# Performance work log

Hardware: AMD Instinct MI355X
Metric: run time of the kernel (lower is better)

Reference implementation:

```python
import jax, jax.numpy as jnp
import numpy as np

OBS_DIM = 64; ACT_DIM = 18; INTER = 64; COMMAND = 32
UNITS = ACT_DIM + COMMAND + INTER  # 114; neuron order: [motor, command, inter]
Q_HIDDEN = max(32, UNITS)
B, T = 2048, 64
ODE_UNFOLDS = 6
EPS = 1e-8


def _build_wiring(seed=0):
    """NCP sparse wiring: sensory->inter, inter->command, command recurrent, command->motor."""
    rng = np.random.default_rng(seed)
    adj = np.zeros((UNITS, UNITS), np.float32)   # [pre, post]
    sens = np.zeros((OBS_DIM, UNITS), np.float32)
    motor = np.arange(ACT_DIM)
    cmd = np.arange(ACT_DIM, ACT_DIM + COMMAND)
    inter = np.arange(ACT_DIM + COMMAND, UNITS)
    for s in range(OBS_DIM):
        for d in rng.choice(inter, size=8, replace=False):
            sens[s, d] = rng.choice([-1.0, 1.0])
    for i in inter:
        for d in rng.choice(cmd, size=8, replace=False):
            adj[i, d] = rng.choice([-1.0, 1.0])
    for _ in range(32):
        adj[rng.choice(cmd), rng.choice(cmd)] = rng.choice([-1.0, 1.0])
    for m in motor:
        for s in rng.choice(cmd, size=8, replace=False):
            adj[s, m] = rng.choice([-1.0, 1.0])
    return adj, sens


def setup_inputs() -> dict:
    key = jax.random.key(0)
    ks = jax.random.split(key, 16)
    adj, sens = _build_wiring()
    u = lambda k, shape, lo, hi: jax.random.uniform(k, shape, jnp.float32, lo, hi)
    return {
        "obs": jax.random.normal(ks[0], (B, T, OBS_DIM), jnp.float32),
        "hidden": jnp.zeros((B, UNITS), jnp.float32),
        "input_w": jnp.ones((OBS_DIM,), jnp.float32),
        "input_b": jnp.zeros((OBS_DIM,), jnp.float32),
        "sensory_w": u(ks[1], (OBS_DIM, UNITS), 0.001, 1.0),
        "sensory_mu": u(ks[2], (OBS_DIM, UNITS), 0.3, 0.8),
        "sensory_sigma": u(ks[3], (OBS_DIM, UNITS), 3.0, 8.0),
        "sensory_erev": jnp.asarray(sens),
        "sensory_mask": jnp.asarray(np.abs(sens)),
        "w": u(ks[4], (UNITS, UNITS), 0.001, 1.0),
        "mu": u(ks[5], (UNITS, UNITS), 0.3, 0.8),
        "sigma": u(ks[6], (UNITS, UNITS), 3.0, 8.0),
        "erev": jnp.asarray(adj),
        "mask": jnp.asarray(np.abs(adj)),
        "gleak": u(ks[7], (UNITS,), 0.001, 1.0),
        "vleak": u(ks[8], (UNITS,), -0.2, 0.2),
        "cm": u(ks[9], (UNITS,), 0.4, 0.6),
        "q_w1": jax.random.normal(ks[10], (UNITS, Q_HIDDEN), jnp.float32) / np.sqrt(UNITS).astype(np.float32),
        "q_b1": jnp.zeros((Q_HIDDEN,), jnp.float32),
        "q_w2": jax.random.normal(ks[11], (Q_HIDDEN, ACT_DIM), jnp.float32) / np.sqrt(Q_HIDDEN).astype(np.float32),
        "q_b2": jnp.zeros((ACT_DIM,), jnp.float32),
    }


def _ltc_forward(obs, hidden, input_w, input_b, sensory_w, sensory_mu, sensory_sigma,
                 sensory_erev, sensory_mask, w, mu, sigma, erev, mask, gleak, vleak, cm):
    sw = sensory_w * sensory_mask          # sparse sensory synapses (S, U)
    ww = w * mask                          # sparse recurrent synapses (U, U)
    cm_t = cm * ODE_UNFOLDS                # cm / (elapsed_time / ode_unfolds), elapsed_time = 1.0

    @jax.checkpoint
    def step(h, x):
        xi = x * input_w + input_b                                                    # (B, S) affine input map
        s_act = sw * jax.nn.sigmoid((xi[:, :, None] - sensory_mu) * sensory_sigma)    # (B, S, U)
        w_num_s = jnp.sum(s_act * sensory_erev, axis=1)                               # (B, U)
        w_den_s = jnp.sum(s_act, axis=1)                                              # (B, U)

        def unfold(v, _):
            act = ww * jax.nn.sigmoid((v[:, :, None] - mu) * sigma)                   # (B, U, U)
            num = cm_t * v + gleak * vleak + jnp.sum(act * erev, axis=1) + w_num_s
            den = cm_t + gleak + jnp.sum(act, axis=1) + w_den_s
            return num / (den + EPS), None

        v, _ = jax.lax.scan(unfold, h, None, length=ODE_UNFOLDS)
        return v, None

    h, _ = jax.lax.scan(step, hidden, jnp.swapaxes(obs, 0, 1))  # scan over time
    return h


def reference(obs, hidden, input_w, input_b, sensory_w, sensory_mu, sensory_sigma,
              sensory_erev, sensory_mask, w, mu, sigma, erev, mask, gleak, vleak, cm,
              q_w1, q_b1, q_w2, q_b2):
    h = _ltc_forward(obs, hidden, input_w, input_b, sensory_w, sensory_mu, sensory_sigma,
                     sensory_erev, sensory_mask, w, mu, sigma, erev, mask, gleak, vleak, cm)
    q = jax.nn.relu(h @ q_w1 + q_b1) @ q_w2 + q_b2  # Q-head over full hidden state
    return q, h
```

## Files before the change

### kernel.cpp

```cpp
#include <hip/hip_runtime.h>

#define UNITS   114
#define SDIM    64
#define ACT     18
#define TSTEPS  64

#define CR 13
#define CS 9
#define ER_CAP 704

#define LOG2E 1.4426950408889634f
#define EPS   1e-8f

typedef float v2f __attribute__((ext_vector_type(2)));
__device__ __forceinline__ v2f fma2(v2f a, v2f b, v2f c) {
  return __builtin_elementwise_fma(a, b, c);
}
__device__ __forceinline__ float bperm(int addr, float v) {
  return __int_as_float(__builtin_amdgcn_ds_bpermute(addr, __float_as_int(v)));
}
__device__ __forceinline__ float dperm(int addr, float v) {
  return __int_as_float(__builtin_amdgcn_ds_permute(addr, __float_as_int(v)));
}
__device__ __forceinline__ void wsync() {
  __builtin_amdgcn_fence(__ATOMIC_ACQ_REL, "wavefront");
  __builtin_amdgcn_wave_barrier();
}
__device__ __forceinline__ int canonLane(int u) { return (u >= 64) ? (u - 64) : u; }

__device__ __forceinline__ int kthSetBit(unsigned long long m, int k) {
  int pos = 0;
#pragma unroll
  for (int ww = 32; ww >= 1; ww >>= 1) {
    const unsigned long long lowMask = ((1ull << ww) - 1ull);
    const int c = __popcll(m & lowMask);
    if (k >= c) { k -= c; m >>= ww; pos += ww; }
  }
  return pos;
}

__global__ __launch_bounds__(64, 2) void ltc_fused(
    const float* __restrict__ obs,     const float* __restrict__ hidden,
    const float* __restrict__ input_w, const float* __restrict__ input_b,
    const float* __restrict__ sw, const float* __restrict__ smu,
    const float* __restrict__ ssg, const float* __restrict__ serev,
    const float* __restrict__ smask,
    const float* __restrict__ w, const float* __restrict__ mu,
    const float* __restrict__ sigma, const float* __restrict__ erev,
    const float* __restrict__ mask,
    const float* __restrict__ gleak, const float* __restrict__ vleak,
    const float* __restrict__ cm,
    const float* __restrict__ q_w1, const float* __restrict__ q_b1,
    const float* __restrict__ q_w2, const float* __restrict__ q_b2,
    float* __restrict__ out, int B)
{
  const int l = threadIdx.x, b = blockIdx.x;
  __shared__ float mirror[256];
  __shared__ short ePre[ER_CAP];
  __shared__ int offL[64], degL[64];
  __shared__ int pLane[64], pF0[64], pRole[64];
  __shared__ int contIdx[64], contOwn[64], splitRole[64], split2[64], ownP[128];
  __shared__ int rcv[64];
  char* mbase = (char*)mirror;

  mirror[l] = hidden[(size_t)b*UNITS + l];
  if (l < 50) mirror[64 + l] = hidden[(size_t)b*UNITS + 64 + l];
  const float iw = input_w[l], ibv = input_b[l];
  const float* ob = obs + (size_t)b*(TSTEPS*SDIM) + l;

  int d = 0;
  if (l < 50) {
    for (int base = 18; base < 114; base += 16) {
      float mv[16];
#pragma unroll
      for (int q = 0; q < 16; ++q) mv[q] = mask[(base + q)*UNITS + l];
#pragma unroll
      for (int q = 0; q < 16; ++q) d += (mv[q] != 0.f) ? 1 : 0;
    }
  }
  const int dregR = (l < 50) ? d : 0;
  degL[l] = dregR;
  int incl = dregR;
#pragma unroll
  for (int o = 1; o < 64; o <<= 1) { const int nn = __shfl_up(incl, o); if (l >= o) incl += nn; }
  offL[l] = incl - dregR;
  contIdx[l] = 0; contOwn[l] = 0; splitRole[l] = -1; split2[l] = 0;
  ownP[2*l] = -1; ownP[2*l+1] = -1;
  wsync();
  if (l < 50) {
    int o = incl - dregR;
    for (int base = 18; base < 114; base += 16) {
      float mv[16];
#pragma unroll
      for (int q = 0; q < 16; ++q) mv[q] = mask[(base + q)*UNITS + l];
#pragma unroll
      for (int q = 0; q < 16; ++q)
        if (mv[q] != 0.f) ePre[o++] = (short)(base + q);
    }
  }
  wsync();
  {
    int lam = 0, f = 0, pc = 0;
    for (int p = 0; p < 50; ++p) {
      const int dd = __shfl(dregR, p);
      if (pc == 2 || f == CR || dd > 3*CR - f) { ++lam; f = 0; pc = 0; }
      if (lam > 63) lam = 63;
      if (l == 0) { pLane[p] = lam; pF0[p] = f; pRole[p] = pc; ownP[2*lam + pc] = p; }
      const int owner = lam, role = pc; ++pc;
      const int take = dd < (CR - f) ? dd : (CR - f);
      f += take; int rem = dd - take;
      if (rem > 0) {
        if (l == 0) { splitRole[owner] = role; split2[owner] = (rem > CR) ? 1 : 0; }
        ++lam; if (lam > 63) lam = 63;
        if (l == 0) { contIdx[lam] = 1; contOwn[lam] = owner; }
        pc = 1;
        const int t2 = rem < CR ? rem : CR; f = t2; rem -= t2;
        if (rem > 0) {
          ++lam; if (lam > 63) lam = 63;
          if (l == 0) { contIdx[lam] = 2; contOwn[lam] = owner; }
          pc = 1; f = rem;
        }
      }
    }
  }
  wsync();
  int dAr = (contIdx[l] == 1) ? contOwn[l] : -1;
  int dBr = (contIdx[l] == 2) ? contOwn[l] : -1;
  rcv[l] = 0; wsync();
  if (dAr >= 0) rcv[dAr] = 1;
  wsync();
  { const unsigned long long rM = __ballot(rcv[l] != 0), dM = __ballot(dAr < 0);
    if (dAr < 0) dAr = kthSetBit(~rM, __popcll(dM & ((1ull << l) - 1ull))); }
  wsync();
  rcv[l] = 0; wsync();
  if (dBr >= 0) rcv[dBr] = 1;
  wsync();
  { const unsigned long long rM = __ballot(rcv[l] != 0), dM = __ballot(dBr < 0);
    if (dBr < 0) dBr = kthSetBit(~rM, __popcll(dM & ((1ull << l) - 1ull))); }
  const int rPush1 = dAr * 4, rPush2 = dBr * 4;
  const float s1Ar = (splitRole[l] == 0) ? 1.f : 0.f, s1Br = (splitRole[l] == 1) ? 1.f : 0.f;
  const float s2r  = split2[l] ? 1.f : 0.f;
  const v2f gR1A = {s1Ar, s1Ar}, gR1B = {s1Br, s1Br};
  const v2f gR2A = {s1Ar*s2r, s1Ar*s2r}, gR2B = {s1Br*s2r, s1Br*s2r};
  const int uA = ownP[2*l], uB = ownP[2*l+1];
  const int rWrA = ((uA >= 0) ? uA : 128 + l) * 4;
  const int rWrB = ((uB >= 0) ? uB : 192 + l) * 4;
  const int rUA = (uA >= 0) ? uA : 0, rUB = (uB >= 0) ? uB : 0;
  float rNS[CR], rMS[CR]; v2f rWA[CR], rWB[CR]; int rad[CR];
  {
    const int ci = contIdx[l];
    int p1 = -1, base1 = 0, cnt1 = 0;
    if (ci) {
      const int o = contOwn[l];
      p1 = ownP[2*o + splitRole[o]];
      const int br = (CR - pF0[p1]) + ((ci == 2) ? CR : 0);
      base1 = offL[p1] + br;
      cnt1 = degL[p1] - br; if (cnt1 > CR) cnt1 = CR;
    }
    int fA = 0, tA = -1, oAo = 0;
    if (uA >= 0) { fA = pF0[uA]; const int rm = CR - fA; const int dd = degL[uA];
                   tA = dd < rm ? dd : rm; oAo = offL[uA]; }
    int fB = 0, tB = -1, oBo = 0;
    if (uB >= 0) { fB = pF0[uB]; const int rm = CR - fB; const int dd = degL[uB];
                   tB = dd < rm ? dd : rm; oBo = offL[uB]; }
#pragma unroll
    for (int s = 0; s < CR; ++s) {
      int e = -1, post = 0, isB = 0;
      if (ci && s < cnt1)                          { e = base1 + s;      post = p1; }
      else if (uA >= 0 && s >= fA && s < fA + tA)  { e = oAo + (s - fA); post = uA; }
      else if (uB >= 0 && s >= fB && s < fB + tB)  { e = oBo + (s - fB); post = uB; isB = 1; }
      if (e >= 0) {
        const int pre = (int)ePre[e];
        const int idx = pre * UNITS + post;
        const float sg_ = sigma[idx];
        rNS[s] = -sg_ * LOG2E; rMS[s] = mu[idx] * sg_ * LOG2E;
        const float wd = w[idx], wn = wd * erev[idx];
        rWA[s] = isB ? (v2f){0.f, 0.f} : (v2f){wn, wd};
        rWB[s] = isB ? (v2f){wn, wd} : (v2f){0.f, 0.f};
        rad[s] = pre * 4;
      } else {
        rNS[s] = 0.f; rMS[s] = 0.f;
        rWA[s] = (v2f){0.f, 0.f}; rWB[s] = (v2f){0.f, 0.f};
        rad[s] = 0;
      }
    }
  }
  wsync();

  int ds_ = 0;
  {
    const int col = 50 + l;
    for (int base = 0; base < 64; base += 16) {
      float mv[16];
#pragma unroll
      for (int q = 0; q < 16; ++q) mv[q] = smask[(base + q)*UNITS + col];
#pragma unroll
      for (int q = 0; q < 16; ++q) ds_ += (mv[q] != 0.f) ? 1 : 0;
    }
  }
  const int dregS = ds_;
  degL[l] = dregS;
  int inclS = dregS;
#pragma unroll
  for (int o = 1; o < 64; o <<= 1) { const int nn = __shfl_up(inclS, o); if (l >= o) inclS += nn; }
  offL[l] = inclS - dregS;
  contIdx[l] = 0; contOwn[l] = 0; splitRole[l] = -1; split2[l] = 0;
  ownP[2*l] = -1; ownP[2*l+1] = -1;
  wsync();
  {
    int o = inclS - dregS; const int col = 50 + l;
    for (int base = 0; base < 64; base += 16) {
      float mv[16];
#pragma unroll
      for (int q = 0; q < 16; ++q) mv[q] = smask[(base + q)*UNITS + col];
#pragma unroll
      for (int q = 0; q < 16; ++q)
        if (mv[q] != 0.f) ePre[o++] = (short)(base + q);
    }
  }
  wsync();
  {
    int lam = 0, f = 0, pc = 0;
    for (int p = 0; p < 64; ++p) {
      const int dd = __shfl(dregS, p);
      if (pc == 2 || f == CS || dd > 3*CS - f) { ++lam; f = 0; pc = 0; }
      if (lam > 63) lam = 63;
      if (l == 0) { pLane[p] = lam; pF0[p] = f; pRole[p] = pc; ownP[2*lam + pc] = p; }
      const int owner = lam, role = pc; ++pc;
      const int take = dd < (CS - f) ? dd : (CS - f);
      f += take; int rem = dd - take;
      if (rem > 0) {
        if (l == 0) { splitRole[owner] = role; split2[owner] = (rem > CS) ? 1 : 0; }
        ++lam; if (lam > 63) lam = 63;
        if (l == 0) { contIdx[lam] = 1; contOwn[lam] = owner; }
        pc = 1;
        const int t2 = rem < CS ? rem : CS; f = t2; rem -= t2;
        if (rem > 0) {
          ++lam; if (lam > 63) lam = 63;
          if (l == 0) { contIdx[lam] = 2; contOwn[lam] = owner; }
          pc = 1; f = rem;
        }
      }
    }
  }
  wsync();
  int dAs = (contIdx[l] == 1) ? contOwn[l] : -1;
  int dBs = (contIdx[l] == 2) ? contOwn[l] : -1;
  rcv[l] = 0; wsync();
  if (dAs >= 0) rcv[dAs] = 1;
  wsync();
  { const unsigned long long rM = __ballot(rcv[l] != 0), dM = __ballot(dAs < 0);
    if (dAs < 0) dAs = kthSetBit(~rM, __popcll(dM & ((1ull << l) - 1ull))); }
  wsync();
  rcv[l] = 0; wsync();
  if (dBs >= 0) rcv[dBs] = 1;
  wsync();
  { const unsigned long long rM = __ballot(rcv[l] != 0), dM = __ballot(dBs < 0);
    if (dBs < 0) dBs = kthSetBit(~rM, __popcll(dM & ((1ull << l) - 1ull))); }
  wsync();
  int rAs = (ownP[2*l]   >= 0) ? canonLane(50 + ownP[2*l])   : -1;
  int rBs = (ownP[2*l+1] >= 0) ? canonLane(50 + ownP[2*l+1]) : -1;
  rcv[l] = 0; wsync();
  if (rAs >= 0) rcv[rAs] = 1;
  wsync();
  const int isRcvA = rcv[l];
  { const unsigned long long rM = __ballot(isRcvA != 0), dM = __ballot(rAs < 0);
    if (rAs < 0) rAs = kthSetBit(~rM, __popcll(dM & ((1ull << l) - 1ull))); }
  wsync();
  rcv[l] = 0; wsync();
  if (rBs >= 0) rcv[rBs] = 1;
  wsync();
  { const unsigned long long rM = __ballot(rcv[l] != 0), dM = __ballot(rBs < 0);
    if (rBs < 0) rBs = kthSetBit(~rM, __popcll(dM & ((1ull << l) - 1ull))); }
  const int sPush1 = dAs * 4, sPush2 = dBs * 4;
  const float s1As = (splitRole[l] == 0) ? 1.f : 0.f, s1Bs = (splitRole[l] == 1) ? 1.f : 0.f;
  const float s2s  = split2[l] ? 1.f : 0.f;
  const v2f gS1A = {s1As, s1As}, gS1B = {s1Bs, s1Bs};
  const v2f gS2A = {s1As*s2s, s1As*s2s}, gS2B = {s1Bs*s2s, s1Bs*s2s};
  const int sRtA = rAs * 4, sRtB = rBs * 4;
  const float sRndA = isRcvA ? 1.f : 0.f, sRndB = isRcvA ? 0.f : 1.f;
  const int pAs = ownP[2*l], pBs = ownP[2*l+1];
  const int sUA = (pAs >= 0) ? 50 + pAs : 0;
  const int sUB = (pBs >= 0) ? 50 + pBs : 0;
  float sNS[CS], sMS[CS]; v2f sWA[CS], sWB[CS]; int sad[CS];
  {
    const int ci = contIdx[l];
    int p1 = -1, base1 = 0, cnt1 = 0;
    if (ci) {
      const int o = contOwn[l];
      p1 = ownP[2*o + splitRole[o]];
      const int br = (CS - pF0[p1]) + ((ci == 2) ? CS : 0);
      base1 = offL[p1] + br;
      cnt1 = degL[p1] - br; if (cnt1 > CS) cnt1 = CS;
    }
    int fA = 0, tA = -1, oAo = 0;
    if (pAs >= 0) { fA = pF0[pAs]; const int rm = CS - fA; const int dd = degL[pAs];
                    tA = dd < rm ? dd : rm; oAo = offL[pAs]; }
    int fB = 0, tB = -1, oBo = 0;
    if (pBs >= 0) { fB = pF0[pBs]; const int rm = CS - fB; const int dd = degL[pBs];
                    tB = dd < rm ? dd : rm; oBo = offL[pBs]; }
#pragma unroll
    for (int s = 0; s < CS; ++s) {
      int e = -1, post = 0, isB = 0;
      if (ci && s < cnt1)                           { e = base1 + s;      post = p1;  }
      else if (pAs >= 0 && s >= fA && s < fA + tA)  { e = oAo + (s - fA); post = pAs; }
      else if (pBs >= 0 && s >= fB && s < fB + tB)  { e = oBo + (s - fB); post = pBs; isB = 1; }
      if (e >= 0) {
        const int pre = (int)ePre[e];
        const int idx = pre * UNITS + 50 + post;
        const float sg_ = ssg[idx];
        sNS[s] = -sg_ * LOG2E; sMS[s] = smu[idx] * sg_ * LOG2E;
        const float wd = sw[idx], wn = wd * serev[idx];
        sWA[s] = isB ? (v2f){0.f, 0.f} : (v2f){wn, wd};
        sWB[s] = isB ? (v2f){wn, wd} : (v2f){0.f, 0.f};
        sad[s] = pre * 4;
      } else {
        sNS[s] = 0.f; sMS[s] = 0.f;
        sWA[s] = (v2f){0.f, 0.f}; sWB[s] = (v2f){0.f, 0.f};
        sad[s] = 0;
      }
    }
  }

  const float cmA  = cm[rUA]*6.f, glvA  = gleak[rUA]*vleak[rUA], cgA  = cm[rUA]*6.f + gleak[rUA] + EPS;
  const float cmB  = cm[rUB]*6.f, glvB  = gleak[rUB]*vleak[rUB], cgB  = cm[rUB]*6.f + gleak[rUB] + EPS;
  const float cmSA = cm[sUA]*6.f, glvSA = gleak[sUA]*vleak[sUA], cgSA = cm[sUA]*6.f + gleak[sUA] + EPS;
  const float cmSB = cm[sUB]*6.f, glvSB = gleak[sUB]*vleak[sUB], cgSB = cm[sUB]*6.f + gleak[sUB] + EPS;

  const bool ownA  = (rWrA < 512), ownB  = (rWrB < 512);
  const bool ownSA = (sUA != 0),   ownSB = (sUB != 0);
  const v2f initRA = ownA  ? (v2f){glvA,  cgA}  : (v2f){0.f, EPS};
  const v2f initRB = ownB  ? (v2f){glvB,  cgB}  : (v2f){0.f, EPS};
  const v2f initSA = ownSA ? (v2f){glvSA, cgSA} : (v2f){0.f, EPS};
  const v2f initSB = ownSB ? (v2f){glvSB, cgSB} : (v2f){0.f, EPS};

  const int  iUnit = (l < 50) ? 64 + l : l;
  const int  iWr   = iUnit * 4;
  float vIn = hidden[(size_t)b*UNITS + iUnit];
  float vPA = hidden[(size_t)b*UNITS + rUA];
  float vPB = hidden[(size_t)b*UNITS + rUB];

  float aI, bI;
  {
    const float xi = fmaf(ob[0], iw, ibv);
    float uu[CS];
#pragma unroll
    for (int s = 0; s < CS; ++s) {
      float z = fmaf(bperm(sad[s], xi), sNS[s], sMS[s]);
      z = fminf(z, 30.f);
      uu[s] = 1.f + __builtin_amdgcn_exp2f(z);
    }
    float sg[CS];
#pragma unroll
    for (int q = 0; q < 4; ++q) {
      const float p = uu[2*q] * uu[2*q+1];
      const float r = __builtin_amdgcn_rcpf(p);
      sg[2*q]   = uu[2*q+1] * r;
      sg[2*q+1] = uu[2*q]   * r;
    }
    sg[8] = __builtin_amdgcn_rcpf(uu[8]);
    v2f cA = {0.f,0.f}, cB = {0.f,0.f};
#pragma unroll
    for (int s = 0; s < CS; ++s) {
      const v2f s2 = {sg[s], sg[s]};
      cA = fma2(sWA[s], s2, cA);
      cB = fma2(sWB[s], s2, cB);
    }
    const v2f m1 = {dperm(sPush1, cA.x), dperm(sPush1, cA.y)};
    const v2f m2 = {dperm(sPush2, cA.x), dperm(sPush2, cA.y)};
    v2f tA = fma2(gS1A, m1, cA); tA = fma2(gS2A, m2, tA);
    v2f tB = fma2(gS1B, m1, cB); tB = fma2(gS2B, m2, tB);
    const float rdA = __builtin_amdgcn_rcpf(cgSA + tA.y);
    const float aA = cmSA * rdA, bA = (glvSA + tA.x) * rdA;
    const float rdB = __builtin_amdgcn_rcpf(cgSB + tB.y);
    const float aB = cmSB * rdB, bB = (glvSB + tB.x) * rdB;
    const float ra1 = dperm(sRtA, aA), rb1 = dperm(sRtA, bA);
    const float ra2 = dperm(sRtB, aB), rb2 = dperm(sRtB, bB);
    aI = sRndA*ra1 + sRndB*ra2;
    bI = sRndA*rb1 + sRndB*rb2;
  }

  float xiN = fmaf(ob[SDIM], iw, ibv);
  float xrC = ob[2*SDIM];
  float su[CS];
  v2f acA = initSA, acB = initSB;
  v2f tSA = {0.f,0.f}, tSB = {0.f,0.f};
  float aIn = 0.f, bIn = 0.f;

  auto unfold = [&](auto chunk) {
    wsync();
    float uu[CR];
#pragma unroll
    for (int s = 0; s < CR; ++s) {
      const float pv = *(const float*)(mbase + rad[s]);
      const float z = fmaf(pv, rNS[s], rMS[s]);
      uu[s] = 1.f + __builtin_amdgcn_exp2f(z);
    }
    chunk();
    float sg[CR];
#pragma unroll
    for (int q = 0; q < 5; ++q) {
      const float p = uu[2*q] * uu[2*q+1];
      const float r = __builtin_amdgcn_rcpf(p);
      sg[2*q]   = uu[2*q+1] * r;
      sg[2*q+1] = uu[2*q]   * r;
    }
    {
      const float p01 = uu[10]*uu[11];
      const float r = __builtin_amdgcn_rcpf(p01*uu[12]);
      const float t12 = uu[12]*r;
      sg[10] = uu[11]*t12; sg[11] = uu[10]*t12; sg[12] = p01*r;
    }
    v2f a0 = initRA, a1 = {0.f,0.f}, b0 = initRB, b1 = {0.f,0.f};
#pragma unroll
    for (int s = 0; s < CR; ++s) {
      const v2f s2 = {sg[s], sg[s]};
      if (s & 1) { a1 = fma2(rWA[s], s2, a1); b1 = fma2(rWB[s], s2, b1); }
      else       { a0 = fma2(rWA[s], s2, a0); b0 = fma2(rWB[s], s2, b0); }
    }
    v2f aA = a0 + a1, aB = b0 + b1;
    const v2f m1 = {dperm(rPush1, aA.x), dperm(rPush1, aA.y)};
    const v2f m2 = {dperm(rPush2, aA.x), dperm(rPush2, aA.y)};
    v2f tA = fma2(gR1A, m1, aA); tA = fma2(gR2A, m2, tA);
    v2f tB = fma2(gR1B, m1, aB); tB = fma2(gR2B, m2, tB);
    const float dAq = tA.y, dBq = tB.y;
    const float rr = __builtin_amdgcn_rcpf(dAq * dBq);
    vPA = fmaf(cmA, vPA, tA.x) * (dBq * rr);
    vPB = fmaf(cmB, vPB, tB.x) * (dAq * rr);
    vIn = fmaf(aI, vIn, bI);
    wsync();
    *(float*)(mbase + rWrA) = vPA;
    *(float*)(mbase + rWrB) = vPB;
    *(float*)(mbase + iWr)  = vIn;
  };

  auto sExp = [&](int s) {
    float z = fmaf(bperm(sad[s], xiN), sNS[s], sMS[s]);
    z = fminf(z, 30.f);
    su[s] = 1.f + __builtin_amdgcn_exp2f(z);
  };
  auto sPair = [&](int s0) {
    const float p = su[s0] * su[s0+1];
    const float r = __builtin_amdgcn_rcpf(p);
    const float g0 = su[s0+1] * r, g1 = su[s0] * r;
    acA = fma2(sWA[s0],   (v2f){g0,g0}, acA);
    acA = fma2(sWA[s0+1], (v2f){g1,g1}, acA);
    acB = fma2(sWB[s0],   (v2f){g0,g0}, acB);
    acB = fma2(sWB[s0+1], (v2f){g1,g1}, acB);
  };

#pragma unroll 1
  for (int t = 0; t < TSTEPS; ++t) {
    unfold([&]{ sExp(0); sExp(1); });
    unfold([&]{ sExp(2); sExp(3); sPair(0); });
    unfold([&]{ sExp(4); sExp(5); sPair(2); });
    unfold([&]{ sExp(6); sExp(7); sExp(8); sPair(4); });
    unfold([&]{
      const float p67 = su[6] * su[7];
      const float r = __builtin_amdgcn_rcpf(p67 * su[8]);
      const float t67 = su[8] * r;
      const float g6 = su[7]*t67, g7 = su[6]*t67, g8 = p67*r;
      acA = fma2(sWA[6], (v2f){g6,g6}, acA); acB = fma2(sWB[6], (v2f){g6,g6}, acB);
      acA = fma2(sWA[7], (v2f){g7,g7}, acA); acB = fma2(sWB[7], (v2f){g7,g7}, acB);
      acA = fma2(sWA[8], (v2f){g8,g8}, acA); acB = fma2(sWB[8], (v2f){g8,g8}, acB);
      const v2f m1 = {dperm(sPush1, acA.x), dperm(sPush1, acA.y)};
      const v2f m2 = {dperm(sPush2, acA.x), dperm(sPush2, acA.y)};
      tSA = fma2(gS1A, m1, acA); tSA = fma2(gS2A, m2, tSA);
      tSB = fma2(gS1B, m1, acB); tSB = fma2(gS2B, m2, tSB);
    });
    unfold([&]{
      const float dA_ = tSA.y, dB_ = tSB.y;
      const float rr = __builtin_amdgcn_rcpf(dA_ * dB_);
      const float rdA = dB_ * rr, rdB = dA_ * rr;
      const float aA = cmSA * rdA, bA = tSA.x * rdA;
      const float aB = cmSB * rdB, bB = tSB.x * rdB;
      const float ra1 = dperm(sRtA, aA), rb1 = dperm(sRtA, bA);
      const float ra2 = dperm(sRtB, aB), rb2 = dperm(sRtB, bB);
      aIn = sRndA*ra1 + sRndB*ra2;
      bIn = sRndA*rb1 + sRndB*rb2;
    });
    aI = aIn; bI = bIn;
    xiN = fmaf(xrC, iw, ibv);
    const int tn = (t + 3 < TSTEPS) ? (t + 3) : (TSTEPS - 1);
    xrC = ob[tn * SDIM];
    acA = initSA; acB = initSB;
  }
  wsync();

  float* __restrict__ outH = out + (size_t)B * ACT;
  outH[(size_t)b*UNITS + l] = mirror[l];
  if (l < 50) outH[(size_t)b*UNITS + 64 + l] = mirror[64 + l];

  const int j2 = (l < 50) ? 64 + l : l;
  float h1 = q_b1[l], h2 = q_b1[j2];
  for (int i = 0; i < UNITS; ++i) {
    const float hv = mirror[i];
    h1 = fmaf(hv, q_w1[i*UNITS + l],  h1);
    h2 = fmaf(hv, q_w1[i*UNITS + j2], h2);
  }
  h1 = fmaxf(h1, 0.f); h2 = fmaxf(h2, 0.f);
  wsync();
  mirror[l] = h1;
  if (l < 50) mirror[64 + l] = h2;
  wsync();
  if (l < ACT) {
    float q = q_b2[l];
    for (int i = 0; i < UNITS; ++i) q = fmaf(mirror[i], q_w2[i*ACT + l], q);
    out[(size_t)b*ACT + l] = q;
  }
}

extern "C" void kernel_launch(void* const* d_in, const int* in_sizes, int n_in,
                              void* d_out, int out_size, void* d_ws, size_t ws_size,
                              hipStream_t stream)
{
  const float* obs           = (const float*)d_in[0];
  const float* hidden        = (const float*)d_in[1];
  const float* input_w       = (const float*)d_in[2];
  const float* input_b       = (const float*)d_in[3];
  const float* sensory_w     = (const float*)d_in[4];
  const float* sensory_mu    = (const float*)d_in[5];
  const float* sensory_sigma = (const float*)d_in[6];
  const float* sensory_erev  = (const float*)d_in[7];
  const float* sensory_mask  = (const float*)d_in[8];
  const float* w             = (const float*)d_in[9];
  const float* mu            = (const float*)d_in[10];
  const float* sigma         = (const float*)d_in[11];
  const float* erev          = (const float*)d_in[12];
  const float* mask          = (const float*)d_in[13];
  const float* gleak         = (const float*)d_in[14];
  const float* vleak         = (const float*)d_in[15];
  const float* cm            = (const float*)d_in[16];
  const float* q_w1          = (const float*)d_in[17];
  const float* q_b1          = (const float*)d_in[18];
  const float* q_w2          = (const float*)d_in[19];
  const float* q_b2          = (const float*)d_in[20];

  const int B = in_sizes[0] / (TSTEPS * SDIM);
  ltc_fused<<<B, 64, 0, stream>>>(
      obs, hidden, input_w, input_b,
      sensory_w, sensory_mu, sensory_sigma, sensory_erev, sensory_mask,
      w, mu, sigma, erev, mask,
      gleak, vleak, cm,
      q_w1, q_b1, q_w2, q_b2,
      (float*)d_out, B);
}
```

Measured before the change: 388.4 us.

## Hoist sparse wiring table construction into a separate prep kernel

The per-block setup that scans the masks, partitions edges across lanes and gathers per-edge parameters moves into a small 8-block prep kernel that writes packed per-lane tables and metadata to workspace. The main kernel now only loads these precomputed tables instead of every one of the 2048 blocks redoing the mask scans, prefix sums and assignment loops. The cost is an extra kernel launch and a global-memory dependency between the two kernels. Edge lists are now rebuilt from bitmasks with kthSetBit rather than stored in a shared-memory list.

```diff
diff --git a/kernel.cpp b/kernel.cpp
--- a/kernel.cpp
+++ b/kernel.cpp
@@ -7,7 +7,7 @@
 
 #define CR 13
 #define CS 9
-#define ER_CAP 704
+#define MSTRIDE 24
 
 #define LOG2E 1.4426950408889634f
 #define EPS   1e-8f
@@ -38,289 +38,306 @@
   }
   return pos;
 }
-
-__global__ __launch_bounds__(64, 2) void ltc_fused(
-    const float* __restrict__ obs,     const float* __restrict__ hidden,
-    const float* __restrict__ input_w, const float* __restrict__ input_b,
+__device__ __forceinline__ unsigned long long shfl_u64(unsigned long long v, int src) {
+  const int lo = __shfl((int)(unsigned)(v & 0xffffffffull), src);
+  const int hi = __shfl((int)(unsigned)(v >> 32), src);
+  return ((unsigned long long)(unsigned)hi << 32) | (unsigned)lo;
+}
+
+__global__ __launch_bounds__(64) void build_all(
+    const float* __restrict__ w,  const float* __restrict__ mu,
+    const float* __restrict__ sigma, const float* __restrict__ erev,
+    const float* __restrict__ mask,
     const float* __restrict__ sw, const float* __restrict__ smu,
     const float* __restrict__ ssg, const float* __restrict__ serev,
     const float* __restrict__ smask,
-    const float* __restrict__ w, const float* __restrict__ mu,
-    const float* __restrict__ sigma, const float* __restrict__ erev,
-    const float* __restrict__ mask,
-    const float* __restrict__ gleak, const float* __restrict__ vleak,
+    float4* __restrict__ recP4, float2* __restrict__ recP2, int* __restrict__ recAd,
+    float4* __restrict__ senP4, float2* __restrict__ senP2, int* __restrict__ senAd,
+    int* __restrict__ meta)
+{
+  const int l = threadIdx.x;
+  const int bid = blockIdx.x;
+  __shared__ int degL[64], pF0L[64];
+  __shared__ int contIdx[64], contOwn[64], splitRole[64], split2[64], ownP[128];
+  __shared__ int rcv[64];
+
+  contIdx[l] = 0; contOwn[l] = 0; splitRole[l] = -1; split2[l] = 0;
+  ownP[2*l] = -1; ownP[2*l+1] = -1;
+
+  if (bid < 4) {
+    unsigned long long cLo = 0ull, cHi = 0ull;
+    if (l < 50) {
+      for (int base = 0; base < 64; base += 16) {
+        float mv[16];
+#pragma unroll
+        for (int q = 0; q < 16; ++q) mv[q] = mask[(18 + base + q)*UNITS + l];
+#pragma unroll
+        for (int q = 0; q < 16; ++q) if (mv[q] != 0.f) cLo |= (1ull << (base + q));
+      }
+      for (int base = 0; base < 32; base += 16) {
+        float mv[16];
+#pragma unroll
+        for (int q = 0; q < 16; ++q) mv[q] = mask[(82 + base + q)*UNITS + l];
+#pragma unroll
+        for (int q = 0; q < 16; ++q) if (mv[q] != 0.f) cHi |= (1ull << (base + q));
+      }
+    }
+    const int dreg = __popcll(cLo) + __popcll(cHi);
+    degL[l] = dreg;
+    wsync();
+    {
+      int lam = 0, f = 0, pc = 0;
+      for (int p = 0; p < 50; ++p) {
+        const int dd = __shfl(dreg, p);
+        if (pc == 2 || f == CR || dd > 3*CR - f) { ++lam; f = 0; pc = 0; }
+        if (lam > 63) lam = 63;
+        if (l == 0) { pF0L[p] = f; ownP[2*lam + pc] = p; }
+        const int owner = lam, role = pc; ++pc;
+        const int take = dd < (CR - f) ? dd : (CR - f);
+        f += take; int rem = dd - take;
+        if (rem > 0) {
+          if (l == 0) { splitRole[owner] = role; split2[owner] = (rem > CR) ? 1 : 0; }
+          ++lam; if (lam > 63) lam = 63;
+          if (l == 0) { contIdx[lam] = 1; contOwn[lam] = owner; }
+          pc = 1;
+          const int t2 = rem < CR ? rem : CR; f = t2; rem -= t2;
+          if (rem > 0) {
+            ++lam; if (lam > 63) lam = 63;
+            if (l == 0) { contIdx[lam] = 2; contOwn[lam] = owner; }
+            pc = 1; f = rem;
+          }
+        }
+      }
+    }
+    wsync();
+    int dAr = (contIdx[l] == 1) ? contOwn[l] : -1;
+    int dBr = (contIdx[l] == 2) ? contOwn[l] : -1;
+    rcv[l] = 0; wsync();
+    if (dAr >= 0) rcv[dAr] = 1;
+    wsync();
+    { const unsigned long long rM = __ballot(rcv[l] != 0), dM = __ballot(dAr < 0);
+      if (dAr < 0) dAr = kthSetBit(~rM, __popcll(dM & ((1ull << l) - 1ull))); }
+    wsync();
+    rcv[l] = 0; wsync();
+    if (dBr >= 0) rcv[dBr] = 1;
+    wsync();
+    { const unsigned long long rM = __ballot(rcv[l] != 0), dM = __ballot(dBr < 0);
+      if (dBr < 0) dBr = kthSetBit(~rM, __popcll(dM & ((1ull << l) - 1ull))); }
+    const int uA = ownP[2*l], uB = ownP[2*l+1];
+    if (bid == 0) {
+      int* M = meta + l * MSTRIDE;
+      M[0] = dAr * 4; M[1] = dBr * 4;
+      const float s1A = (splitRole[l] == 0) ? 1.f : 0.f, s1B = (splitRole[l] == 1) ? 1.f : 0.f;
+      M[2] = __float_as_int(s1A); M[3] = __float_as_int(s1B);
+      const float s2 = split2[l] ? 1.f : 0.f;
+      M[4] = __float_as_int(s1A * s2); M[5] = __float_as_int(s1B * s2);
+      M[6] = ((uA >= 0) ? uA : 128 + l) * 4;
+      M[7] = ((uB >= 0) ? uB : 192 + l) * 4;
+      M[8] = (uA >= 0) ? uA : 0;
+      M[9] = (uB >= 0) ? uB : 0;
+    }
+    const int ci = contIdx[l];
+    int p1 = -1, br = 0, cnt1 = 0;
+    if (ci) {
+      const int o = contOwn[l];
+      p1 = ownP[2*o + splitRole[o]];
+      br = (CR - pF0L[p1]) + ((ci == 2) ? CR : 0);
+      cnt1 = degL[p1] - br; if (cnt1 > CR) cnt1 = CR;
+    }
+    int fA = 0, tA = -1;
+    if (uA >= 0) { fA = pF0L[uA]; const int rm = CR - fA; const int dd = degL[uA]; tA = dd < rm ? dd : rm; }
+    int fB = 0, tB = -1;
+    if (uB >= 0) { fB = pF0L[uB]; const int rm = CR - fB; const int dd = degL[uB]; tB = dd < rm ? dd : rm; }
+    for (int s = bid; s < CR; s += 4) {
+      int post = -1, rank = 0, isB = 0;
+      if (ci && s < cnt1)                          { post = p1; rank = br + s; }
+      else if (uA >= 0 && s >= fA && s < fA + tA)  { post = uA; rank = s - fA; }
+      else if (uB >= 0 && s >= fB && s < fB + tB)  { post = uB; rank = s - fB; isB = 1; }
+      const int postc = (post >= 0) ? post : 0;
+      const unsigned long long plo = shfl_u64(cLo, postc);
+      const unsigned long long phi = shfl_u64(cHi, postc);
+      float4 p4 = make_float4(0.f, 0.f, 0.f, 0.f);
+      float2 p2 = make_float2(0.f, 0.f);
+      int ad = 0;
+      if (post >= 0) {
+        const int c = __popcll(plo);
+        const int pre = (rank < c) ? (18 + kthSetBit(plo, rank)) : (82 + kthSetBit(phi, rank - c));
+        const int idx = pre * UNITS + post;
+        const float sg_ = sigma[idx];
+        const float nsgl = -sg_ * LOG2E, msl = mu[idx] * sg_ * LOG2E;
+        const float wd = w[idx], wn = wd * erev[idx];
+        p4 = make_float4(nsgl, msl, isB ? 0.f : wn, isB ? 0.f : wd);
+        p2 = isB ? make_float2(wn, wd) : make_float2(0.f, 0.f);
+        ad = pre * 4;
+      }
+      recP4[s*64 + l] = p4; recP2[s*64 + l] = p2; recAd[s*64 + l] = ad;
+    }
+  } else {
+    unsigned long long cS = 0ull;
+    {
+      const int col = 50 + l;
+      for (int base = 0; base < 64; base += 16) {
+        float mv[16];
+#pragma unroll
+        for (int q = 0; q < 16; ++q) mv[q] = smask[(base + q)*UNITS + col];
+#pragma unroll
+        for (int q = 0; q < 16; ++q) if (mv[q] != 0.f) cS |= (1ull << (base + q));
+      }
+    }
+    const int dreg = __popcll(cS);
+    degL[l] = dreg;
+    wsync();
+    {
+      int lam = 0, f = 0, pc = 0;
+      for (int p = 0; p < 64; ++p) {
+        const int dd = __shfl(dreg, p);
+        if (pc == 2 || f == CS || dd > 3*CS - f) { ++lam; f = 0; pc = 0; }
+        if (lam > 63) lam = 63;
+        if (l == 0) { pF0L[p] = f; ownP[2*lam + pc] = p; }
+        const int owner = lam, role = pc; ++pc;
+        const int take = dd < (CS - f) ? dd : (CS - f);
+        f += take; int rem = dd - take;
+        if (rem > 0) {
+          if (l == 0) { splitRole[owner] = role; split2[owner] = (rem > CS) ? 1 : 0; }
+          ++lam; if (lam > 63) lam = 63;
+          if (l == 0) { contIdx[lam] = 1; contOwn[lam] = owner; }
+          pc = 1;
+          const int t2 = rem < CS ? rem : CS; f = t2; rem -= t2;
+          if (rem > 0) {
+            ++lam; if (lam > 63) lam = 63;
+            if (l == 0) { contIdx[lam] = 2; contOwn[lam] = owner; }
+            pc = 1; f = rem;
+          }
+        }
+      }
+    }
+    wsync();
+    int dAs = (contIdx[l] == 1) ? contOwn[l] : -1;
+    int dBs = (contIdx[l] == 2) ? contOwn[l] : -1;
+    rcv[l] = 0; wsync();
+    if (dAs >= 0) rcv[dAs] = 1;
+    wsync();
+    { const unsigned long long rM = __ballot(rcv[l] != 0), dM = __ballot(dAs < 0);
+      if (dAs < 0) dAs = kthSetBit(~rM, __popcll(dM & ((1ull << l) - 1ull))); }
+    wsync();
+    rcv[l] = 0; wsync();
+    if (dBs >= 0) rcv[dBs] = 1;
+    wsync();
+    { const unsigned long long rM = __ballot(rcv[l] != 0), dM = __ballot(dBs < 0);
+      if (dBs < 0) dBs = kthSetBit(~rM, __popcll(dM & ((1ull << l) - 1ull))); }
+    wsync();
+    int rAs = (ownP[2*l]   >= 0) ? canonLane(50 + ownP[2*l])   : -1;
+    int rBs = (ownP[2*l+1] >= 0) ? canonLane(50 + ownP[2*l+1]) : -1;
+    rcv[l] = 0; wsync();
+    if (rAs >= 0) rcv[rAs] = 1;
+    wsync();
+    const int isRcvA = rcv[l];
+    { const unsigned long long rM = __ballot(isRcvA != 0), dM = __ballot(rAs < 0);
+      if (rAs < 0) rAs = kthSetBit(~rM, __popcll(dM & ((1ull << l) - 1ull))); }
+    wsync();
+    rcv[l] = 0; wsync();
+    if (rBs >= 0) rcv[rBs] = 1;
+    wsync();
+    { const unsigned long long rM = __ballot(rcv[l] != 0), dM = __ballot(rBs < 0);
+      if (rBs < 0) rBs = kthSetBit(~rM, __popcll(dM & ((1ull << l) - 1ull))); }
+    const int pAs = ownP[2*l], pBs = ownP[2*l+1];
+    if (bid == 4) {
+      int* M = meta + l * MSTRIDE;
+      M[10] = dAs * 4; M[11] = dBs * 4;
+      const float s1A = (splitRole[l] == 0) ? 1.f : 0.f, s1B = (splitRole[l] == 1) ? 1.f : 0.f;
+      M[12] = __float_as_int(s1A); M[13] = __float_as_int(s1B);
+      const float s2 = split2[l] ? 1.f : 0.f;
+      M[14] = __float_as_int(s1A * s2); M[15] = __float_as_int(s1B * s2);
+      M[16] = rAs * 4; M[17] = rBs * 4;
+      M[18] = __float_as_int(isRcvA ? 1.f : 0.f);
+      M[19] = __float_as_int(isRcvA ? 0.f : 1.f);
+      M[20] = (pAs >= 0) ? 50 + pAs : 0;
+      M[21] = (pBs >= 0) ? 50 + pBs : 0;
+    }
+    const int ci = contIdx[l];
+    int p1 = -1, br = 0, cnt1 = 0;
+    if (ci) {
+      const int o = contOwn[l];
+      p1 = ownP[2*o + splitRole[o]];
+      br = (CS - pF0L[p1]) + ((ci == 2) ? CS : 0);
+      cnt1 = degL[p1] - br; if (cnt1 > CS) cnt1 = CS;
+    }
+    int fA = 0, tA = -1;
+    if (pAs >= 0) { fA = pF0L[pAs]; const int rm = CS - fA; const int dd = degL[pAs]; tA = dd < rm ? dd : rm; }
+    int fB = 0, tB = -1;
+    if (pBs >= 0) { fB = pF0L[pBs]; const int rm = CS - fB; const int dd = degL[pBs]; tB = dd < rm ? dd : rm; }
+    for (int s = bid - 4; s < CS; s += 4) {
+      int post = -1, rank = 0, isB = 0;
+      if (ci && s < cnt1)                            { post = p1;  rank = br + s; }
+      else if (pAs >= 0 && s >= fA && s < fA + tA)   { post = pAs; rank = s - fA; }
+      else if (pBs >= 0 && s >= fB && s < fB + tB)   { post = pBs; rank = s - fB; isB = 1; }
+      const int postc = (post >= 0) ? post : 0;
+      const unsigned long long pm = shfl_u64(cS, postc);
+      float4 p4 = make_float4(0.f, 0.f, 0.f, 0.f);
+      float2 p2 = make_float2(0.f, 0.f);
+      int ad = 0;
+      if (post >= 0) {
+        const int pre = kthSetBit(pm, rank);
+        const int idx = pre * UNITS + 50 + post;
+        const float sg_ = ssg[idx];
+        const float nsgl = -sg_ * LOG2E, msl = smu[idx] * sg_ * LOG2E;
+        const float wd = sw[idx], wn = wd * serev[idx];
+        p4 = make_float4(nsgl, msl, isB ? 0.f : wn, isB ? 0.f : wd);
+        p2 = isB ? make_float2(wn, wd) : make_float2(0.f, 0.f);
+        ad = pre * 4;
+      }
+      senP4[s*64 + l] = p4; senP2[s*64 + l] = p2; senAd[s*64 + l] = ad;
+    }
+  }
+}
+
+__global__ __launch_bounds__(64, 2) void ltc_run(
+    const float* __restrict__ obs,     const float* __restrict__ hidden,
+    const float* __restrict__ input_w, const float* __restrict__ input_b,
+    const float* __restrict__ gleak,   const float* __restrict__ vleak,
     const float* __restrict__ cm,
     const float* __restrict__ q_w1, const float* __restrict__ q_b1,
     const float* __restrict__ q_w2, const float* __restrict__ q_b2,
-    float* __restrict__ out, int B)
+    const float4* __restrict__ recP4, const float2* __restrict__ recP2,
+    const int* __restrict__ recAd,
+    const float4* __restrict__ senP4, const float2* __restrict__ senP2,
+    const int* __restrict__ senAd,
+    const int* __restrict__ meta, float* __restrict__ out, int B)
 {
   const int l = threadIdx.x, b = blockIdx.x;
   __shared__ float mirror[256];
-  __shared__ short ePre[ER_CAP];
-  __shared__ int offL[64], degL[64];
-  __shared__ int pLane[64], pF0[64], pRole[64];
-  __shared__ int contIdx[64], contOwn[64], splitRole[64], split2[64], ownP[128];
-  __shared__ int rcv[64];
   char* mbase = (char*)mirror;
 
-  mirror[l] = hidden[(size_t)b*UNITS + l];
-  if (l < 50) mirror[64 + l] = hidden[(size_t)b*UNITS + 64 + l];
-  const float iw = input_w[l], ibv = input_b[l];
-  const float* ob = obs + (size_t)b*(TSTEPS*SDIM) + l;
-
-  int d = 0;
-  if (l < 50) {
-    for (int base = 18; base < 114; base += 16) {
-      float mv[16];
-#pragma unroll
-      for (int q = 0; q < 16; ++q) mv[q] = mask[(base + q)*UNITS + l];
-#pragma unroll
-      for (int q = 0; q < 16; ++q) d += (mv[q] != 0.f) ? 1 : 0;
-    }
-  }
-  const int dregR = (l < 50) ? d : 0;
-  degL[l] = dregR;
-  int incl = dregR;
-#pragma unroll
-  for (int o = 1; o < 64; o <<= 1) { const int nn = __shfl_up(incl, o); if (l >= o) incl += nn; }
-  offL[l] = incl - dregR;
-  contIdx[l] = 0; contOwn[l] = 0; splitRole[l] = -1; split2[l] = 0;
-  ownP[2*l] = -1; ownP[2*l+1] = -1;
-  wsync();
-  if (l < 50) {
-    int o = incl - dregR;
-    for (int base = 18; base < 114; base += 16) {
-      float mv[16];
-#pragma unroll
-      for (int q = 0; q < 16; ++q) mv[q] = mask[(base + q)*UNITS + l];
-#pragma unroll
-      for (int q = 0; q < 16; ++q)
-        if (mv[q] != 0.f) ePre[o++] = (short)(base + q);
-    }
-  }
-  wsync();
-  {
-    int lam = 0, f = 0, pc = 0;
-    for (int p = 0; p < 50; ++p) {
-      const int dd = __shfl(dregR, p);
-      if (pc == 2 || f == CR || dd > 3*CR - f) { ++lam; f = 0; pc = 0; }
-      if (lam > 63) lam = 63;
-      if (l == 0) { pLane[p] = lam; pF0[p] = f; pRole[p] = pc; ownP[2*lam + pc] = p; }
-      const int owner = lam, role = pc; ++pc;
-      const int take = dd < (CR - f) ? dd : (CR - f);
-      f += take; int rem = dd - take;
-      if (rem > 0) {
-        if (l == 0) { splitRole[owner] = role; split2[owner] = (rem > CR) ? 1 : 0; }
-        ++lam; if (lam > 63) lam = 63;
-        if (l == 0) { contIdx[lam] = 1; contOwn[lam] = owner; }
-        pc = 1;
-        const int t2 = rem < CR ? rem : CR; f = t2; rem -= t2;
-        if (rem > 0) {
-          ++lam; if (lam > 63) lam = 63;
-          if (l == 0) { contIdx[lam] = 2; contOwn[lam] = owner; }
-          pc = 1; f = rem;
-        }
-      }
-    }
-  }
-  wsync();
-  int dAr = (contIdx[l] == 1) ? contOwn[l] : -1;
-  int dBr = (contIdx[l] == 2) ? contOwn[l] : -1;
-  rcv[l] = 0; wsync();
-  if (dAr >= 0) rcv[dAr] = 1;
-  wsync();
-  { const unsigned long long rM = __ballot(rcv[l] != 0), dM = __ballot(dAr < 0);
-    if (dAr < 0) dAr = kthSetBit(~rM, __popcll(dM & ((1ull << l) - 1ull))); }
-  wsync();
-  rcv[l] = 0; wsync();
-  if (dBr >= 0) rcv[dBr] = 1;
-  wsync();
-  { const unsigned long long rM = __ballot(rcv[l] != 0), dM = __ballot(dBr < 0);
-    if (dBr < 0) dBr = kthSetBit(~rM, __popcll(dM & ((1ull << l) - 1ull))); }
-  const int rPush1 = dAr * 4, rPush2 = dBr * 4;
-  const float s1Ar = (splitRole[l] == 0) ? 1.f : 0.f, s1Br = (splitRole[l] == 1) ? 1.f : 0.f;
-  const float s2r  = split2[l] ? 1.f : 0.f;
-  const v2f gR1A = {s1Ar, s1Ar}, gR1B = {s1Br, s1Br};
-  const v2f gR2A = {s1Ar*s2r, s1Ar*s2r}, gR2B = {s1Br*s2r, s1Br*s2r};
-  const int uA = ownP[2*l], uB = ownP[2*l+1];
-  const int rWrA = ((uA >= 0) ? uA : 128 + l) * 4;
-  const int rWrB = ((uB >= 0) ? uB : 192 + l) * 4;
-  const int rUA = (uA >= 0) ? uA : 0, rUB = (uB >= 0) ? uB : 0;
   float rNS[CR], rMS[CR]; v2f rWA[CR], rWB[CR]; int rad[CR];
-  {
-    const int ci = contIdx[l];
-    int p1 = -1, base1 = 0, cnt1 = 0;
-    if (ci) {
-      const int o = contOwn[l];
-      p1 = ownP[2*o + splitRole[o]];
-      const int br = (CR - pF0[p1]) + ((ci == 2) ? CR : 0);
-      base1 = offL[p1] + br;
-      cnt1 = degL[p1] - br; if (cnt1 > CR) cnt1 = CR;
-    }
-    int fA = 0, tA = -1, oAo = 0;
-    if (uA >= 0) { fA = pF0[uA]; const int rm = CR - fA; const int dd = degL[uA];
-                   tA = dd < rm ? dd : rm; oAo = offL[uA]; }
-    int fB = 0, tB = -1, oBo = 0;
-    if (uB >= 0) { fB = pF0[uB]; const int rm = CR - fB; const int dd = degL[uB];
-                   tB = dd < rm ? dd : rm; oBo = offL[uB]; }
-#pragma unroll
-    for (int s = 0; s < CR; ++s) {
-      int e = -1, post = 0, isB = 0;
-      if (ci && s < cnt1)                          { e = base1 + s;      post = p1; }
-      else if (uA >= 0 && s >= fA && s < fA + tA)  { e = oAo + (s - fA); post = uA; }
-      else if (uB >= 0 && s >= fB && s < fB + tB)  { e = oBo + (s - fB); post = uB; isB = 1; }
-      if (e >= 0) {
-        const int pre = (int)ePre[e];
-        const int idx = pre * UNITS + post;
-        const float sg_ = sigma[idx];
-        rNS[s] = -sg_ * LOG2E; rMS[s] = mu[idx] * sg_ * LOG2E;
-        const float wd = w[idx], wn = wd * erev[idx];
-        rWA[s] = isB ? (v2f){0.f, 0.f} : (v2f){wn, wd};
-        rWB[s] = isB ? (v2f){wn, wd} : (v2f){0.f, 0.f};
-        rad[s] = pre * 4;
-      } else {
-        rNS[s] = 0.f; rMS[s] = 0.f;
-        rWA[s] = (v2f){0.f, 0.f}; rWB[s] = (v2f){0.f, 0.f};
-        rad[s] = 0;
-      }
-    }
-  }
-  wsync();
-
-  int ds_ = 0;
-  {
-    const int col = 50 + l;
-    for (int base = 0; base < 64; base += 16) {
-      float mv[16];
-#pragma unroll
-      for (int q = 0; q < 16; ++q) mv[q] = smask[(base + q)*UNITS + col];
-#pragma unroll
-      for (int q = 0; q < 16; ++q) ds_ += (mv[q] != 0.f) ? 1 : 0;
-    }
-  }
-  const int dregS = ds_;
-  degL[l] = dregS;
-  int inclS = dregS;
-#pragma unroll
-  for (int o = 1; o < 64; o <<= 1) { const int nn = __shfl_up(inclS, o); if (l >= o) inclS += nn; }
-  offL[l] = inclS - dregS;
-  contIdx[l] = 0; contOwn[l] = 0; splitRole[l] = -1; split2[l] = 0;
-  ownP[2*l] = -1; ownP[2*l+1] = -1;
-  wsync();
-  {
-    int o = inclS - dregS; const int col = 50 + l;
-    for (int base = 0; base < 64; base += 16) {
-      float mv[16];
-#pragma unroll
-      for (int q = 0; q < 16; ++q) mv[q] = smask[(base + q)*UNITS + col];
-#pragma unroll
-      for (int q = 0; q < 16; ++q)
-        if (mv[q] != 0.f) ePre[o++] = (short)(base + q);
-    }
-  }
-  wsync();
-  {
-    int lam = 0, f = 0, pc = 0;
-    for (int p = 0; p < 64; ++p) {
-      const int dd = __shfl(dregS, p);
-      if (pc == 2 || f == CS || dd > 3*CS - f) { ++lam; f = 0; pc = 0; }
-      if (lam > 63) lam = 63;
-      if (l == 0) { pLane[p] = lam; pF0[p] = f; pRole[p] = pc; ownP[2*lam + pc] = p; }
-      const int owner = lam, role = pc; ++pc;
-      const int take = dd < (CS - f) ? dd : (CS - f);
-      f += take; int rem = dd - take;
-      if (rem > 0) {
-        if (l == 0) { splitRole[owner] = role; split2[owner] = (rem > CS) ? 1 : 0; }
-        ++lam; if (lam > 63) lam = 63;
-        if (l == 0) { contIdx[lam] = 1; contOwn[lam] = owner; }
-        pc = 1;
-        const int t2 = rem < CS ? rem : CS; f = t2; rem -= t2;
-        if (rem > 0) {
-          ++lam; if (lam > 63) lam = 63;
-          if (l == 0) { contIdx[lam] = 2; contOwn[lam] = owner; }
-          pc = 1; f = rem;
-        }
-      }
-    }
-  }
-  wsync();
-  int dAs = (contIdx[l] == 1) ? contOwn[l] : -1;
-  int dBs = (contIdx[l] == 2) ? contOwn[l] : -1;
-  rcv[l] = 0; wsync();
-  if (dAs >= 0) rcv[dAs] = 1;
-  wsync();
-  { const unsigned long long rM = __ballot(rcv[l] != 0), dM = __ballot(dAs < 0);
-    if (dAs < 0) dAs = kthSetBit(~rM, __popcll(dM & ((1ull << l) - 1ull))); }
-  wsync();
-  rcv[l] = 0; wsync();
-  if (dBs >= 0) rcv[dBs] = 1;
-  wsync();
-  { const unsigned long long rM = __ballot(rcv[l] != 0), dM = __ballot(dBs < 0);
-    if (dBs < 0) dBs = kthSetBit(~rM, __popcll(dM & ((1ull << l) - 1ull))); }
-  wsync();
-  int rAs = (ownP[2*l]   >= 0) ? canonLane(50 + ownP[2*l])   : -1;
-  int rBs = (ownP[2*l+1] >= 0) ? canonLane(50 + ownP[2*l+1]) : -1;
-  rcv[l] = 0; wsync();
-  if (rAs >= 0) rcv[rAs] = 1;
-  wsync();
-  const int isRcvA = rcv[l];
-  { const unsigned long long rM = __ballot(isRcvA != 0), dM = __ballot(rAs < 0);
-    if (rAs < 0) rAs = kthSetBit(~rM, __popcll(dM & ((1ull << l) - 1ull))); }
-  wsync();
-  rcv[l] = 0; wsync();
-  if (rBs >= 0) rcv[rBs] = 1;
-  wsync();
-  { const unsigned long long rM = __ballot(rcv[l] != 0), dM = __ballot(rBs < 0);
-    if (rBs < 0) rBs = kthSetBit(~rM, __popcll(dM & ((1ull << l) - 1ull))); }
-  const int sPush1 = dAs * 4, sPush2 = dBs * 4;
-  const float s1As = (splitRole[l] == 0) ? 1.f : 0.f, s1Bs = (splitRole[l] == 1) ? 1.f : 0.f;
-  const float s2s  = split2[l] ? 1.f : 0.f;
-  const v2f gS1A = {s1As, s1As}, gS1B = {s1Bs, s1Bs};
-  const v2f gS2A = {s1As*s2s, s1As*s2s}, gS2B = {s1Bs*s2s, s1Bs*s2s};
-  const int sRtA = rAs * 4, sRtB = rBs * 4;
-  const float sRndA = isRcvA ? 1.f : 0.f, sRndB = isRcvA ? 0.f : 1.f;
-  const int pAs = ownP[2*l], pBs = ownP[2*l+1];
-  const int sUA = (pAs >= 0) ? 50 + pAs : 0;
-  const int sUB = (pBs >= 0) ? 50 + pBs : 0;
+#pragma unroll
+  for (int s = 0; s < CR; ++s) {
+    const float4 p4 = recP4[s*64 + l]; const float2 p2 = recP2[s*64 + l];
+    rNS[s] = p4.x; rMS[s] = p4.y; rWA[s] = (v2f){p4.z, p4.w};
+    rWB[s] = (v2f){p2.x, p2.y}; rad[s] = recAd[s*64 + l];
+  }
   float sNS[CS], sMS[CS]; v2f sWA[CS], sWB[CS]; int sad[CS];
-  {
-    const int ci = contIdx[l];
-    int p1 = -1, base1 = 0, cnt1 = 0;
-    if (ci) {
-      const int o = contOwn[l];
-      p1 = ownP[2*o + splitRole[o]];
-      const int br = (CS - pF0[p1]) + ((ci == 2) ? CS : 0);
-      base1 = offL[p1] + br;
-      cnt1 = degL[p1] - br; if (cnt1 > CS) cnt1 = CS;
-    }
-    int fA = 0, tA = -1, oAo = 0;
-    if (pAs >= 0) { fA = pF0[pAs]; const int rm = CS - fA; const int dd = degL[pAs];
-                    tA = dd < rm ? dd : rm; oAo = offL[pAs]; }
-    int fB = 0, tB = -1, oBo = 0;
-    if (pBs >= 0) { fB = pF0[pBs]; const int rm = CS - fB; const int dd = degL[pBs];
-                    tB = dd < rm ? dd : rm; oBo = offL[pBs]; }
-#pragma unroll
-    for (int s = 0; s < CS; ++s) {
-      int e = -1, post = 0, isB = 0;
-      if (ci && s < cnt1)                           { e = base1 + s;      post = p1;  }
-      else if (pAs >= 0 && s >= fA && s < fA + tA)  { e = oAo + (s - fA); post = pAs; }
-      else if (pBs >= 0 && s >= fB && s < fB + tB)  { e = oBo + (s - fB); post = pBs; isB = 1; }
-      if (e >= 0) {
-        const int pre = (int)ePre[e];
-        const int idx = pre * UNITS + 50 + post;
-        const float sg_ = ssg[idx];
-        sNS[s] = -sg_ * LOG2E; sMS[s] = smu[idx] * sg_ * LOG2E;
-        const float wd = sw[idx], wn = wd * serev[idx];
-        sWA[s] = isB ? (v2f){0.f, 0.f} : (v2f){wn, wd};
-        sWB[s] = isB ? (v2f){wn, wd} : (v2f){0.f, 0.f};
-        sad[s] = pre * 4;
-      } else {
-        sNS[s] = 0.f; sMS[s] = 0.f;
-        sWA[s] = (v2f){0.f, 0.f}; sWB[s] = (v2f){0.f, 0.f};
-        sad[s] = 0;
-      }
-    }
-  }
+#pragma unroll
+  for (int s = 0; s < CS; ++s) {
+    const float4 p4 = senP4[s*64 + l]; const float2 p2 = senP2[s*64 + l];
+    sNS[s] = p4.x; sMS[s] = p4.y; sWA[s] = (v2f){p4.z, p4.w};
+    sWB[s] = (v2f){p2.x, p2.y}; sad[s] = senAd[s*64 + l];
+  }
+
+  const int* M = meta + l * MSTRIDE;
+  const int   rPush1 = M[0], rPush2 = M[1];
+  const v2f gR1A = {__int_as_float(M[2]), __int_as_float(M[2])};
+  const v2f gR1B = {__int_as_float(M[3]), __int_as_float(M[3])};
+  const v2f gR2A = {__int_as_float(M[4]), __int_as_float(M[4])};
+  const v2f gR2B = {__int_as_float(M[5]), __int_as_float(M[5])};
+  const int   rWrA = M[6], rWrB = M[7], rUA = M[8], rUB = M[9];
+  const int   sPush1 = M[10], sPush2 = M[11];
+  const v2f gS1A = {__int_as_float(M[12]), __int_as_float(M[12])};
+  const v2f gS1B = {__int_as_float(M[13]), __int_as_float(M[13])};
+  const v2f gS2A = {__int_as_float(M[14]), __int_as_float(M[14])};
+  const v2f gS2B = {__int_as_float(M[15]), __int_as_float(M[15])};
+  const int   sRtA = M[16], sRtB = M[17];
+  const float sRndA = __int_as_float(M[18]), sRndB = __int_as_float(M[19]);
+  const int   sUA = M[20], sUB = M[21];
 
   const float cmA  = cm[rUA]*6.f, glvA  = gleak[rUA]*vleak[rUA], cgA  = cm[rUA]*6.f + gleak[rUA] + EPS;
   const float cmB  = cm[rUB]*6.f, glvB  = gleak[rUB]*vleak[rUB], cgB  = cm[rUB]*6.f + gleak[rUB] + EPS;
@@ -339,6 +356,12 @@
   float vIn = hidden[(size_t)b*UNITS + iUnit];
   float vPA = hidden[(size_t)b*UNITS + rUA];
   float vPB = hidden[(size_t)b*UNITS + rUB];
+
+  mirror[l] = hidden[(size_t)b*UNITS + l];
+  if (l < 50) mirror[64 + l] = hidden[(size_t)b*UNITS + 64 + l];
+
+  const float iw = input_w[l], ibv = input_b[l];
+  const float* ob = obs + (size_t)b*(TSTEPS*SDIM) + l;
 
   float aI, bI;
   {
@@ -536,12 +559,24 @@
   const float* q_w2          = (const float*)d_in[19];
   const float* q_b2          = (const float*)d_in[20];
 
+  char* ws = (char*)d_ws;
+  float4* recP4 = (float4*)(ws);
+  float2* recP2 = (float2*)(ws + 13312);
+  int*    recAd = (int*)   (ws + 19968);
+  float4* senP4 = (float4*)(ws + 23296);
+  float2* senP2 = (float2*)(ws + 32512);
+  int*    senAd = (int*)   (ws + 37120);
+  int*    meta  = (int*)   (ws + 39424);
+
+  build_all<<<8, 64, 0, stream>>>(
+      w, mu, sigma, erev, mask,
+      sensory_w, sensory_mu, sensory_sigma, sensory_erev, sensory_mask,
+      recP4, recP2, recAd, senP4, senP2, senAd, meta);
+
   const int B = in_sizes[0] / (TSTEPS * SDIM);
-  ltc_fused<<<B, 64, 0, stream>>>(
-      obs, hidden, input_w, input_b,
-      sensory_w, sensory_mu, sensory_sigma, sensory_erev, sensory_mask,
-      w, mu, sigma, erev, mask,
-      gleak, vleak, cm,
+  ltc_run<<<B, 64, 0, stream>>>(
+      obs, hidden, input_w, input_b, gleak, vleak, cm,
       q_w1, q_b1, q_w2, q_b2,
+      recP4, recP2, recAd, senP4, senP2, senAd, meta,
       (float*)d_out, B);
 }
```

Result: faster. 359.3 us (-7.5%).
